# Kernel optimization log

Measured on AMD Instinct MI355X. Metric: run time of the kernel, lower is better.

Reference implementation:

```python
import jax, jax.numpy as jnp
import numpy as np

D_MODEL = 768
N_HEADS = 12
HEAD_DIM = D_MODEL // N_HEADS
FFN_DIM = 3072
MAX_WAVELENGTH = 10000.0
ROPE_PERCENT = 0.5
NORM_EPS = 1e-5


def setup_inputs() -> dict:
    key = jax.random.key(0)
    ks = jax.random.split(key, 12)
    B, C, S = 2, 16, 128
    init = lambda k, shape: (jax.random.normal(k, shape, dtype=jnp.float32) * 0.02)
    return {
        "hidden_state": jax.random.normal(ks[0], (B, C, S, D_MODEL), dtype=jnp.float32),
        "wq": init(ks[1], (D_MODEL, D_MODEL)), "bq": jnp.zeros((D_MODEL,), jnp.float32),
        "wk": init(ks[2], (D_MODEL, D_MODEL)), "bk": jnp.zeros((D_MODEL,), jnp.float32),
        "wv": init(ks[3], (D_MODEL, D_MODEL)), "bv": jnp.zeros((D_MODEL,), jnp.float32),
        "wo": init(ks[4], (D_MODEL, D_MODEL)), "bo": jnp.zeros((D_MODEL,), jnp.float32),
        "attn_biases": init(ks[5], (N_HEADS, 2)),
        "ln1_g": jnp.ones((D_MODEL,), jnp.float32), "ln1_b": jnp.zeros((D_MODEL,), jnp.float32),
        "ln3_g": jnp.ones((D_MODEL,), jnp.float32), "ln3_b": jnp.zeros((D_MODEL,), jnp.float32),
        "w1": init(ks[6], (D_MODEL, FFN_DIM)), "b1": jnp.zeros((FFN_DIM,), jnp.float32),
        "w2": init(ks[7], (FFN_DIM, D_MODEL)), "b2": jnp.zeros((D_MODEL,), jnp.float32),
    }


def _layernorm(x, g, b):
    mu = jnp.mean(x, axis=-1, keepdims=True)
    var = jnp.mean(jnp.square(x - mu), axis=-1, keepdims=True)
    return (x - mu) * jax.lax.rsqrt(var + NORM_EPS) * g + b


def _apply_p_rope(x, positions):
    # x: [B, H, T, head_dim]; p-RoPE: only rope_percent of frequency bands rotate.
    half = HEAD_DIM // 2
    rope_angles = int(ROPE_PERCENT * HEAD_DIM) // 2  # 16
    fraction = 2.0 * jnp.arange(rope_angles, dtype=jnp.float32) / HEAD_DIM
    timescale = jnp.concatenate([
        MAX_WAVELENGTH ** fraction,
        jnp.full((half - rope_angles,), jnp.inf, dtype=jnp.float32),
    ])  # [half]
    angles = positions[:, None].astype(jnp.float32) / timescale[None, :]  # [T, half]
    sin = jnp.sin(angles)[None, None]  # [1,1,T,half]
    cos = jnp.cos(angles)[None, None]
    x1, x2 = jnp.split(x, 2, axis=-1)
    return jnp.concatenate([x1 * cos - x2 * sin, x2 * cos + x1 * sin], axis=-1)


def _forward(hidden_state, wq, bq, wk, bk, wv, bv, wo, bo, attn_biases,
             ln1_g, ln1_b, ln3_g, ln3_b, w1, b1, w2, b2):
    B, C, S, D = hidden_state.shape
    T = C * S
    flat = hidden_state.reshape(B, T, D)

    # --- attention sublayer (pre-norm) ---
    ni = _layernorm(flat, ln1_g, ln1_b)
    scaling = HEAD_DIM ** -0.5
    q = (ni @ wq + bq) * scaling
    k = ni @ wk + bk
    v = ni @ wv + bv
    to_heads = lambda t: t.reshape(B, T, N_HEADS, HEAD_DIM).transpose(0, 2, 1, 3)
    q, k, v = to_heads(q), to_heads(k), to_heads(v)  # [B,H,T,hd]

    positions = jnp.arange(T)
    k = _apply_p_rope(k, positions)
    q = _apply_p_rope(q, positions)

    scores = jnp.einsum("bhtd,bhsd->bhts", q, k)  # [B,H,T,T]
    variate_ids = positions // S
    same = (variate_ids[:, None] == variate_ids[None, :]).astype(scores.dtype)  # [T,T]
    variate_bias = (same[None, :, :] * attn_biases[:, 0][:, None, None]
                    + (1.0 - same[None, :, :]) * attn_biases[:, 1][:, None, None])  # [H,T,T]
    scores = scores + variate_bias[None]
    probs = jax.nn.softmax(scores, axis=-1)
    attn = jnp.einsum("bhts,bhsd->bhtd", probs, v)
    attn = attn.transpose(0, 2, 1, 3).reshape(B, T, D)
    attn = attn @ wo + bo

    flat = flat + attn  # residual (pre-norm -> no post-norm here)

    # --- feed-forward sublayer (pre-norm) ---
    ff_in = _layernorm(flat, ln3_g, ln3_b)
    ff = jax.nn.gelu(ff_in @ w1 + b1, approximate=False) @ w2 + b2
    flat = flat + ff

    return flat.reshape(B, C, S, D)


def reference(hidden_state, wq, bq, wk, bk, wv, bv, wo, bo, attn_biases,
              ln1_g, ln1_b, ln3_g, ln3_b, w1, b1, w2, b2):
    return _forward(hidden_state, wq, bq, wk, bk, wv, bv, wo, bo, attn_biases,
                    ln1_g, ln1_b, ln3_g, ln3_b, w1, b1, w2, b2)
```

## Files before the change

### kernel.cpp

```cpp
#include <hip/hip_runtime.h>
#include <cmath>


typedef __bf16 bf16_t;
typedef bf16_t bf16x8 __attribute__((ext_vector_type(8)));
typedef float floatx4 __attribute__((ext_vector_type(4)));
typedef unsigned int u32x4 __attribute__((ext_vector_type(4)));

#define MFMA(a, b, c) __builtin_amdgcn_mfma_f32_16x16x32_bf16((a), (b), (c), 0, 0, 0)
#define LOG2E 1.44269504088896340736f

__device__ __forceinline__ bf16_t f2bf(float f) { return (bf16_t)f; }

__device__ __forceinline__ void g2l16(const void* g, void* l) {
  __builtin_amdgcn_global_load_lds(
      (const __attribute__((address_space(1))) unsigned int*)g,
      (__attribute__((address_space(3))) unsigned int*)l, 16, 0, 0);
}

__device__ __forceinline__ void wait_vm4() {
  asm volatile("s_waitcnt vmcnt(4)" ::: "memory");
}
__device__ __forceinline__ void wait_vm0() {
  asm volatile("s_waitcnt vmcnt(0)" ::: "memory");
}

__device__ __forceinline__ unsigned cvt_pk_bf16(float lo, float hi) {
  unsigned r;
  asm("v_cvt_pk_bf16_f32 %0, %1, %2" : "=v"(r) : "v"(lo), "v"(hi));
  return r;
}
__device__ __forceinline__ void pl32swap(unsigned& a, unsigned& b) {
  asm("v_permlane32_swap_b32 %0, %1" : "+v"(a), "+v"(b));
}
__device__ __forceinline__ void pl16swap(unsigned& a, unsigned& b) {
  asm("v_permlane16_swap_b32 %0, %1" : "+v"(a), "+v"(b));
}

struct PrepP {
  const float *wq, *wk, *wv, *wo, *w1, *w2;
  bf16_t *wqkvT, *woT, *w1T, *w2T;
  const float *hs, *g1, *be1;
  bf16_t* ni;
};

__global__ __launch_bounds__(256) void k_prep(PrepP p) {
  __shared__ float shm[32 * 33];
  const int bid = blockIdx.x;
  if (bid < 6912) {
    const float* in;
    bf16_t* out;
    int R, C, tx, ty;
    if (bid < 2304) {
      int m = bid / 576, lo = bid % 576;
      in = (m == 0) ? p.wq : (m == 1) ? p.wk : (m == 2) ? p.wv : p.wo;
      out = (m < 3) ? p.wqkvT + (size_t)m * 768 * 768 : p.woT;
      R = 768; C = 768; tx = lo % 24; ty = lo / 24;
    } else if (bid < 4608) {
      int lo = bid - 2304;
      in = p.w1; out = p.w1T; R = 768; C = 3072; tx = lo % 96; ty = lo / 96;
    } else {
      int lo = bid - 4608;
      in = p.w2; out = p.w2T; R = 3072; C = 768; tx = lo % 24; ty = lo / 24;
    }
    const int c0 = tx * 32, r0 = ty * 32;
    const int lx = threadIdx.x & 31, ly = threadIdx.x >> 5;
#pragma unroll
    for (int p4 = 0; p4 < 4; p4++) {
      int r = ly + p4 * 8;
      shm[r * 33 + lx] = in[(size_t)(r0 + r) * C + c0 + lx];
    }
    __syncthreads();
#pragma unroll
    for (int p4 = 0; p4 < 4; p4++) {
      int r = ly + p4 * 8;
      out[(size_t)(c0 + r) * R + r0 + lx] = f2bf(shm[lx * 33 + r]);
    }
  } else {
    const int row = bid - 6912;
    const float* xr = p.hs + (size_t)row * 768;
    const int t = threadIdx.x;
    float v0 = xr[t], v1 = xr[t + 256], v2 = xr[t + 512];
    float s = v0 + v1 + v2;
    float s2 = v0 * v0 + v1 * v1 + v2 * v2;
#pragma unroll
    for (int off = 32; off; off >>= 1) {
      s += __shfl_xor(s, off);
      s2 += __shfl_xor(s2, off);
    }
    const int w = t >> 6;
    if ((t & 63) == 0) { shm[w] = s; shm[4 + w] = s2; }
    __syncthreads();
    s = shm[0] + shm[1] + shm[2] + shm[3];
    s2 = shm[4] + shm[5] + shm[6] + shm[7];
    const float mu = s * (1.0f / 768.0f);
    const float var = s2 * (1.0f / 768.0f) - mu * mu;
    const float rstd = rsqrtf(var + 1e-5f);
    bf16_t* orow = p.ni + (size_t)row * 768;
    orow[t]       = f2bf((v0 - mu) * rstd * p.g1[t]       + p.be1[t]);
    orow[t + 256] = f2bf((v1 - mu) * rstd * p.g1[t + 256] + p.be1[t + 256]);
    orow[t + 512] = f2bf((v2 - mu) * rstd * p.g1[t + 512] + p.be1[t + 512]);
  }
}

__global__ __launch_bounds__(256) void k_layernorm(
    const float* __restrict__ x, const float* __restrict__ g,
    const float* __restrict__ b, bf16_t* __restrict__ out) {
  const int row = blockIdx.x;
  const float* xr = x + (size_t)row * 768;
  const int t = threadIdx.x;
  float v0 = xr[t], v1 = xr[t + 256], v2 = xr[t + 512];
  float s = v0 + v1 + v2;
  float s2 = v0 * v0 + v1 * v1 + v2 * v2;
#pragma unroll
  for (int off = 32; off; off >>= 1) {
    s += __shfl_xor(s, off);
    s2 += __shfl_xor(s2, off);
  }
  __shared__ float ra[4], rb[4];
  const int w = t >> 6;
  if ((t & 63) == 0) { ra[w] = s; rb[w] = s2; }
  __syncthreads();
  s = ra[0] + ra[1] + ra[2] + ra[3];
  s2 = rb[0] + rb[1] + rb[2] + rb[3];
  const float mu = s * (1.0f / 768.0f);
  const float var = s2 * (1.0f / 768.0f) - mu * mu;
  const float rstd = rsqrtf(var + 1e-5f);
  bf16_t* orow = out + (size_t)row * 768;
  orow[t]       = f2bf((v0 - mu) * rstd * g[t]       + b[t]);
  orow[t + 256] = f2bf((v1 - mu) * rstd * g[t + 256] + b[t + 256]);
  orow[t + 512] = f2bf((v2 - mu) * rstd * g[t + 512] + b[t + 512]);
}

struct GemmP {
  const bf16_t* A;
  const bf16_t* Bt;
  int M, N, K, mode;
  const float* bias0;
  const float* bias1;
  const float* bias2;
  float* outF;
  bf16_t* outB0;
  bf16_t* outB1;
  bf16_t* outB2;
};

__global__ __launch_bounds__(256, 3) void k_gemm(GemmP p) {
  __shared__ bf16_t lds[18432];
  const int tid = threadIdx.x;
  const int lane = tid & 63, wave = tid >> 6;
  const int quad = lane >> 4, l15 = lane & 15;
  const int wm = (wave >> 1) * 64, wn = (wave & 1) * 64;
  const int m0 = blockIdx.y * 128, n0 = blockIdx.x * 128;

  const char* gA[4];
  const char* gB[4];
#pragma unroll
  for (int pp = 0; pp < 4; pp++) {
    int slot = wave * 256 + pp * 64 + lane;
    int r = slot >> 3;
    int c8 = ((slot & 7) ^ (r & 7)) << 3;
    gA[pp] = (const char*)(p.A + (size_t)(m0 + r) * p.K + c8);
    gB[pp] = (const char*)(p.Bt + (size_t)(n0 + r) * p.K + c8);
  }

  int offA[4], offB[4];
#pragma unroll
  for (int i = 0; i < 4; i++) {
    int ra = wm + i * 16 + l15;
    offA[i] = ra * 64 + ((quad * 8) ^ ((ra & 7) << 3));
    int rb = wn + i * 16 + l15;
    offB[i] = rb * 64 + ((quad * 8) ^ ((rb & 7) << 3));
  }

  const floatx4 z4 = {0.f, 0.f, 0.f, 0.f};
  floatx4 acc[4][4];
#pragma unroll
  for (int i = 0; i < 4; i++)
#pragma unroll
    for (int j = 0; j < 4; j++) acc[i][j] = z4;

  const int KT = p.K >> 6;
  bf16_t* Ad = lds + wave * 2048;
  bf16_t* Bd = lds + 8192 + wave * 2048;

  for (int kt = 0; kt < KT; kt++) {
    const size_t kb = (size_t)kt * 128;
#pragma unroll
    for (int pp = 0; pp < 4; pp++) {
      g2l16(gA[pp] + kb, Ad + pp * 512);
      g2l16(gB[pp] + kb, Bd + pp * 512);
    }
    __syncthreads();
#pragma unroll
    for (int ks = 0; ks < 2; ks++) {
      bf16x8 af[4], bfr[4];
#pragma unroll
      for (int i = 0; i < 4; i++) {
        af[i] = *(const bf16x8*)(lds + (offA[i] ^ (ks * 32)));
        bfr[i] = *(const bf16x8*)(lds + 8192 + (offB[i] ^ (ks * 32)));
      }
#pragma unroll
      for (int i = 0; i < 4; i++)
#pragma unroll
        for (int j = 0; j < 4; j++) acc[i][j] = MFMA(af[i], bfr[j], acc[i][j]);
    }
    __syncthreads();
  }

  char* scr = (char*)lds + wave * 9216;

  if (p.mode == 0) {
    const int gnw = n0 + wn;
    const int region = gnw / 768;
    const int rem = gnw - region * 768;
    const int h = rem >> 6;
    const int b = (m0 + wm) >> 11;
    const int t0 = (m0 + wm) & 2047;
    const float* bias = (region == 0) ? p.bias0 : (region == 1 ? p.bias1 : p.bias2);
    float bb[4];
#pragma unroll
    for (int j = 0; j < 4; j++) bb[j] = bias[h * 64 + j * 16 + l15];
    bf16_t* sb = (bf16_t*)scr;
    if (region < 2) {
      const float scale = (region == 0) ? 0.125f * LOG2E : 1.0f;
      const float inv_ts = exp2f(-(float)l15 * (13.287712379549449f / 32.0f));
#pragma unroll
      for (int i = 0; i < 4; i++) {
#pragma unroll
        for (int reg = 0; reg < 4; reg++) {
          int tl = i * 16 + quad * 4 + reg;
          float sn, cs;
          __sincosf((float)(t0 + tl) * inv_ts, &sn, &cs);
          float v0 = (acc[i][0][reg] + bb[0]) * scale;
          float v1 = (acc[i][1][reg] + bb[1]) * scale;
          float v2 = (acc[i][2][reg] + bb[2]) * scale;
          float v3 = (acc[i][3][reg] + bb[3]) * scale;
          sb[tl * 72 + l15]      = f2bf(v0 * cs - v2 * sn);
          sb[tl * 72 + 16 + l15] = f2bf(v1);
          sb[tl * 72 + 32 + l15] = f2bf(v2 * cs + v0 * sn);
          sb[tl * 72 + 48 + l15] = f2bf(v3);
        }
      }
      __syncthreads();
      bf16_t* outp = (region == 0) ? p.outB0 : p.outB1;
      bf16_t* ob = outp + (((size_t)(b * 12 + h) * 2048 + t0) << 6);
#pragma unroll
      for (int pp = 0; pp < 8; pp++) {
        int row = pp * 8 + (lane >> 3), ch = (lane & 7) << 3;
        *(bf16x8*)(ob + row * 64 + ch) = *(const bf16x8*)&sb[row * 72 + ch];
      }
    } else {
#pragma unroll
      for (int i = 0; i < 4; i++)
#pragma unroll
        for (int j = 0; j < 4; j++)
#pragma unroll
          for (int reg = 0; reg < 4; reg++)
            sb[(j * 16 + l15) * 72 + i * 16 + quad * 4 + reg] =
                f2bf(acc[i][j][reg] + bb[j]);
      __syncthreads();
      bf16_t* ob = p.outB2 + (((size_t)(b * 12 + h)) << 17) + t0;
#pragma unroll
      for (int pp = 0; pp < 8; pp++) {
        int d = pp * 8 + (lane >> 3), ch = (lane & 7) << 3;
        *(bf16x8*)(ob + (size_t)d * 2048 + ch) = *(const bf16x8*)&sb[d * 72 + ch];
      }
    }
  } else {
    bf16_t* sb = (bf16_t*)scr;
    float bb[4];
#pragma unroll
    for (int j = 0; j < 4; j++) bb[j] = p.bias0[n0 + wn + j * 16 + l15];
#pragma unroll
    for (int i = 0; i < 4; i++)
#pragma unroll
      for (int j = 0; j < 4; j++)
#pragma unroll
        for (int reg = 0; reg < 4; reg++) {
          int tl = i * 16 + quad * 4 + reg;
          float x = acc[i][j][reg] + bb[j];
          float gv = 0.5f * x * (1.0f + erff(x * 0.70710678118654752f));
          sb[tl * 72 + j * 16 + l15] = f2bf(gv);
        }
    __syncthreads();
#pragma unroll
    for (int pp = 0; pp < 8; pp++) {
      int row = pp * 8 + (lane >> 3), ch = (lane & 7) << 3;
      *(bf16x8*)(p.outB0 + (size_t)(m0 + wm + row) * p.N + n0 + wn + ch) =
          *(const bf16x8*)&sb[row * 72 + ch];
    }
  }
}

__global__ __launch_bounds__(256, 4) void k_gemm64(
    const bf16_t* __restrict__ A, const bf16_t* __restrict__ Bt, int N, int K,
    const float* __restrict__ bias, const float* __restrict__ resid,
    float* __restrict__ outF) {
  __shared__ bf16_t lds[16384];
  const int tid = threadIdx.x;
  const int lane = tid & 63, wave = tid >> 6;
  const int quad = lane >> 4, l15 = lane & 15;
  const int wm = (wave >> 1) * 32, wn = (wave & 1) * 32;
  const int m0 = blockIdx.y * 64, n0 = blockIdx.x * 64;

  const char* gA[4];
  const char* gB[4];
#pragma unroll
  for (int pp = 0; pp < 4; pp++) {
    int slot = wave * 256 + pp * 64 + lane;
    int r = slot >> 4;
    int c = ((slot & 15) ^ (r & 7)) << 3;
    gA[pp] = (const char*)(A + (size_t)(m0 + r) * K + c);
    gB[pp] = (const char*)(Bt + (size_t)(n0 + r) * K + c);
  }

  const floatx4 z4 = {0.f, 0.f, 0.f, 0.f};
  floatx4 acc[2][2];
#pragma unroll
  for (int i = 0; i < 2; i++)
#pragma unroll
    for (int j = 0; j < 2; j++) acc[i][j] = z4;

  const int KT = K >> 7;
  bf16_t* Ad = lds + wave * 2048;
  bf16_t* Bd = lds + 8192 + wave * 2048;

  for (int kt = 0; kt < KT; kt++) {
    const size_t kb = (size_t)kt * 256;
#pragma unroll
    for (int pp = 0; pp < 4; pp++) {
      g2l16(gA[pp] + kb, Ad + pp * 512);
      g2l16(gB[pp] + kb, Bd + pp * 512);
    }
    __syncthreads();
#pragma unroll
    for (int ks = 0; ks < 4; ks++) {
      bf16x8 af[2], bfr[2];
#pragma unroll
      for (int i = 0; i < 2; i++) {
        int ra = wm + i * 16 + l15;
        af[i] = *(const bf16x8*)(lds + ra * 128 +
                                 (((ks * 4 + quad) ^ (ra & 7)) << 3));
        int rb = wn + i * 16 + l15;
        bfr[i] = *(const bf16x8*)(lds + 8192 + rb * 128 +
                                  (((ks * 4 + quad) ^ (rb & 7)) << 3));
      }
#pragma unroll
      for (int i = 0; i < 2; i++)
#pragma unroll
        for (int j = 0; j < 2; j++) acc[i][j] = MFMA(af[i], bfr[j], acc[i][j]);
    }
    __syncthreads();
  }

  float* s4 = (float*)lds + wave * 1024;
#pragma unroll
  for (int i = 0; i < 2; i++)
#pragma unroll
    for (int j = 0; j < 2; j++)
#pragma unroll
      for (int reg = 0; reg < 4; reg++)
        s4[(i * 16 + quad * 4 + reg) * 32 + j * 16 + l15] = acc[i][j][reg];
  __syncthreads();
#pragma unroll
  for (int pp = 0; pp < 4; pp++) {
    int row = pp * 8 + (lane >> 3);
    int c4 = (lane & 7) * 4;
    floatx4 v = *(const floatx4*)&s4[row * 32 + c4];
    size_t goff = (size_t)(m0 + wm + row) * N + n0 + wn + c4;
    floatx4 rv = *(const floatx4*)(resid + goff);
    floatx4 bv = *(const floatx4*)(bias + n0 + wn + c4);
    *(floatx4*)(outF + goff) = v + rv + bv;
  }
}

__global__ __launch_bounds__(256, 3) void k_flash(
    const bf16_t* __restrict__ qh, const bf16_t* __restrict__ kh,
    const bf16_t* __restrict__ vt, const float* __restrict__ ab,
    bf16_t* __restrict__ attnA) {
  __shared__ bf16_t sm[25088];

  const int tid = threadIdx.x, lane = tid & 63, wave = tid >> 6;
  const int quad = lane >> 4, l15 = lane & 15;
  const int qtile = blockIdx.x, bh = blockIdx.y;
  const int h = bh % 12, bq = bh / 12;
  const int myv = qtile >> 1;

  bf16_t* wb = sm + wave * 6144;
  bf16_t* Kb0 = wb;
  bf16_t* Vs = wb + 2048;

  const bf16_t* Qg = qh + ((size_t)bh * 2048 + qtile * 64) * 64;
  const bf16_t* Kg = kh + ((size_t)bh * 2048 + wave * 16) * 64;

  const char* gK[2];
#pragma unroll
  for (int i = 0; i < 2; i++) {
    int sl = i * 8 + (lane >> 3);
    int cs = (lane & 7) ^ (sl & 7);
    gK[i] = (const char*)(Kg + sl * 64 + cs * 8);
  }
  const char* gV[2];
#pragma unroll
  for (int i = 0; i < 2; i++) {
    int d = i * 32 + (lane >> 1);
    int hs = (lane & 1) ^ ((d >> 2) & 1);
    gV[i] = (const char*)(vt + ((size_t)(bh * 64 + d)) * 2048 + wave * 16 + hs * 8);
  }

  bf16x8 qf[4][2];
#pragma unroll
  for (int mt = 0; mt < 4; mt++)
#pragma unroll
    for (int ks = 0; ks < 2; ks++)
      qf[mt][ks] = *(const bf16x8*)(Qg + (size_t)(mt * 16 + l15) * 64 +
                                    ks * 32 + quad * 8);

  int offKr[2];
#pragma unroll
  for (int ks = 0; ks < 2; ks++)
    offKr[ks] = l15 * 64 + ((((ks << 2) + quad) ^ (l15 & 7)) << 3);
  int offV[4];
#pragma unroll
  for (int nt = 0; nt < 4; nt++) {
    int d = nt * 16 + l15;
    offV[nt] = (quad >> 1) * 1024 + d * 16 +
               (((quad & 1) ^ ((d >> 2) & 1)) << 3);
  }

  const floatx4 z4 = {0.f, 0.f, 0.f, 0.f};
  floatx4 oacc[4][4];
  float l_mt[4];
  unsigned pA[4], pB[4];
#pragma unroll
  for (int mt = 0; mt < 4; mt++)
#pragma unroll
    for (int nt = 0; nt < 4; nt++) oacc[mt][nt] = z4;
#pragma unroll
  for (int mt = 0; mt < 4; mt++) l_mt[mt] = 0.f;

  const float bc_same = ab[h * 2] * LOG2E;
  const float bc_diff = ab[h * 2 + 1] * LOG2E;

  g2l16(gK[0], Kb0);
  g2l16(gK[1], Kb0 + 512);
  g2l16(gV[0], Vs);
  g2l16(gV[1], Vs + 512);

#pragma unroll 2
  for (int kv = 0; kv < 32; kv++) {
    const int nkv = (kv + 1) & 31;
    {
      const size_t kbK = (size_t)nkv * 8192, kbV = (size_t)nkv * 128;
      bf16_t* Kd = Kb0 + (nkv & 1) * 1024;
      bf16_t* Vd = Vs + ((((nkv >> 1) & 1) << 1) + (nkv & 1)) * 1024;
      g2l16(gK[0] + kbK, Kd);
      g2l16(gK[1] + kbK, Kd + 512);
      g2l16(gV[0] + kbV, Vd);
      g2l16(gV[1] + kbV, Vd + 512);
    }
    wait_vm4();

    const bf16_t* Kc = Kb0 + (kv & 1) * 1024;
    const float bc = ((kv >> 1) == myv) ? bc_same : bc_diff;
    floatx4 sacc[4];
#pragma unroll
    for (int mt = 0; mt < 4; mt++) sacc[mt] = (floatx4){bc, bc, bc, bc};
#pragma unroll
    for (int ks = 0; ks < 2; ks++) {
      const bf16x8 kf = *(const bf16x8*)(Kc + offKr[ks]);
#pragma unroll
      for (int mt = 0; mt < 4; mt++)
        sacc[mt] = MFMA(kf, qf[mt][ks], sacc[mt]);
    }

    if (!(kv & 1)) {
#pragma unroll
      for (int mt = 0; mt < 4; mt++) {
        float p0 = exp2f(sacc[mt][0]), p1 = exp2f(sacc[mt][1]);
        float p2 = exp2f(sacc[mt][2]), p3 = exp2f(sacc[mt][3]);
        l_mt[mt] += (p0 + p1) + (p2 + p3);
        pA[mt] = cvt_pk_bf16(p0, p1);
        pB[mt] = cvt_pk_bf16(p2, p3);
      }
    } else {
      bf16x8 vf[4];
      const int vb = ((kv >> 1) & 1) * 2048;
#pragma unroll
      for (int nt = 0; nt < 4; nt++)
        vf[nt] = *(const bf16x8*)(Vs + vb + offV[nt]);
#pragma unroll
      for (int mt = 0; mt < 4; mt++) {
        float p0 = exp2f(sacc[mt][0]), p1 = exp2f(sacc[mt][1]);
        float p2 = exp2f(sacc[mt][2]), p3 = exp2f(sacc[mt][3]);
        l_mt[mt] += (p0 + p1) + (p2 + p3);
        unsigned b0 = cvt_pk_bf16(p0, p1);
        unsigned b1 = cvt_pk_bf16(p2, p3);
        unsigned a0 = pA[mt], a1 = pB[mt];
        pl32swap(a0, b0);
        pl16swap(a0, b0);
        pl32swap(a1, b1);
        pl16swap(a1, b1);
        u32x4 w;
        w[0] = a0; w[1] = a1; w[2] = b0; w[3] = b1;
        const bf16x8 pf = __builtin_bit_cast(bf16x8, w);
#pragma unroll
        for (int nt = 0; nt < 4; nt++)
          oacc[mt][nt] = MFMA(pf, vf[nt], oacc[mt][nt]);
      }
    }
  }

  wait_vm0();

#pragma unroll
  for (int mt = 0; mt < 4; mt++) {
    float v = l_mt[mt];
    v += __shfl_xor(v, 16);
    v += __shfl_xor(v, 32);
    l_mt[mt] = v;
  }
  float* lred = (float*)(sm + 24576);
  if (quad == 0) {
#pragma unroll
    for (int mt = 0; mt < 4; mt++)
      lred[wave * 64 + mt * 16 + l15] = l_mt[mt];
  }
#pragma unroll
  for (int mt = 0; mt < 4; mt++)
#pragma unroll
    for (int nt = 0; nt < 4; nt++)
#pragma unroll
      for (int reg = 0; reg < 4; reg++)
        wb[(mt * 16 + quad * 4 + reg) * 64 + nt * 16 + l15] =
            f2bf(oacc[mt][nt][reg]);
  __syncthreads();

  const int q = tid >> 2, dg = (tid & 3) * 16;
  const float inv =
      1.0f / (lred[q] + lred[64 + q] + lred[128 + q] + lred[192 + q]);
  float o[16];
#pragma unroll
  for (int j = 0; j < 16; j++) o[j] = 0.f;
#pragma unroll
  for (int w = 0; w < 4; w++) {
    const bf16x8 a = *(const bf16x8*)(sm + w * 6144 + q * 64 + dg);
    const bf16x8 b = *(const bf16x8*)(sm + w * 6144 + q * 64 + dg + 8);
#pragma unroll
    for (int j = 0; j < 8; j++) {
      o[j] += (float)a[j];
      o[8 + j] += (float)b[j];
    }
  }
  bf16x8 r0, r1;
#pragma unroll
  for (int j = 0; j < 8; j++) {
    r0[j] = f2bf(o[j] * inv);
    r1[j] = f2bf(o[8 + j] * inv);
  }
  bf16_t* outp =
      attnA + ((size_t)(bq * 2048 + qtile * 64 + q)) * 768 + h * 64 + dg;
  *(bf16x8*)outp = r0;
  *(bf16x8*)(outp + 8) = r1;
}

extern "C" void kernel_launch(void* const* d_in, const int* in_sizes, int n_in,
                              void* d_out, int out_size, void* d_ws,
                              size_t ws_size, hipStream_t stream) {
  const float* hs  = (const float*)d_in[0];
  const float* wq  = (const float*)d_in[1];
  const float* bq  = (const float*)d_in[2];
  const float* wk  = (const float*)d_in[3];
  const float* bk  = (const float*)d_in[4];
  const float* wv  = (const float*)d_in[5];
  const float* bv  = (const float*)d_in[6];
  const float* wo  = (const float*)d_in[7];
  const float* bo  = (const float*)d_in[8];
  const float* ab  = (const float*)d_in[9];
  const float* g1  = (const float*)d_in[10];
  const float* be1 = (const float*)d_in[11];
  const float* g3  = (const float*)d_in[12];
  const float* be3 = (const float*)d_in[13];
  const float* w1  = (const float*)d_in[14];
  const float* b1  = (const float*)d_in[15];
  const float* w2  = (const float*)d_in[16];
  const float* b2  = (const float*)d_in[17];

  char* ws = (char*)d_ws;
  size_t off = 0;
  auto alloc = [&](size_t bytes) -> void* {
    void* p = ws + off;
    off += (bytes + 255) & ~(size_t)255;
    return p;
  };
  bf16_t* wqkvT = (bf16_t*)alloc((size_t)2304 * 768 * 2);
  bf16_t* woT   = (bf16_t*)alloc((size_t)768 * 768 * 2);
  bf16_t* w1T   = (bf16_t*)alloc((size_t)3072 * 768 * 2);
  bf16_t* w2T   = (bf16_t*)alloc((size_t)768 * 3072 * 2);
  bf16_t* ni    = (bf16_t*)alloc((size_t)4096 * 768 * 2);
  bf16_t* qhB   = (bf16_t*)alloc((size_t)24 * 2048 * 64 * 2);
  bf16_t* khB   = (bf16_t*)alloc((size_t)24 * 2048 * 64 * 2);
  bf16_t* vtB   = (bf16_t*)alloc((size_t)24 * 64 * 2048 * 2);
  bf16_t* attnA = (bf16_t*)alloc((size_t)4096 * 768 * 2);
  float*  resid1 = (float*)alloc((size_t)4096 * 768 * 4);
  bf16_t* ffn1o = qhB;

  PrepP pp = {wq, wk, wv, wo, w1, w2, wqkvT, woT, w1T, w2T, hs, g1, be1, ni};
  k_prep<<<11008, 256, 0, stream>>>(pp);

  GemmP gqkv = {ni, wqkvT, 4096, 2304, 768, 0,
                bq, bk, bv, nullptr, qhB, khB, vtB};
  k_gemm<<<dim3(18, 32), 256, 0, stream>>>(gqkv);

  k_flash<<<dim3(32, 24), 256, 0, stream>>>(qhB, khB, vtB, ab, attnA);

  k_gemm64<<<dim3(12, 64), 256, 0, stream>>>(attnA, woT, 768, 768, bo, hs,
                                             resid1);

  k_layernorm<<<4096, 256, 0, stream>>>(resid1, g3, be3, ni);

  GemmP gf1 = {ni, w1T, 4096, 3072, 768, 2,
               b1, nullptr, nullptr, nullptr, ffn1o, nullptr, nullptr};
  k_gemm<<<dim3(24, 32), 256, 0, stream>>>(gf1);

  k_gemm64<<<dim3(12, 64), 256, 0, stream>>>(ffn1o, w2T, 768, 3072, b2,
                                             resid1, (float*)d_out);
}
```

Baseline: 269.2 us.

## Load V fragments directly to registers and deepen K prefetch in flash kernel

The flash-attention kernel stops staging V through LDS. Each wave now loads V fragments straight from global memory into double-buffered registers one pair-iteration ahead, while K is prefetched two steps ahead in a four-slot LDS ring. The variate bias is restructured to initialize scores with the cross-variate bias and multiply by a precomputed exp2 ratio on same-variate tiles, and it uses the raw hardware exp2 builtin. Less LDS per block may allow higher occupancy, but the change adds register pressure and exposes direct global-load latency for V.

```diff
diff --git a/kernel.cpp b/kernel.cpp
--- a/kernel.cpp
+++ b/kernel.cpp
@@ -12,14 +12,18 @@
 
 __device__ __forceinline__ bf16_t f2bf(float f) { return (bf16_t)f; }
 
+__device__ __forceinline__ float fexp2(float x) {
+  return __builtin_amdgcn_exp2f(x);
+}
+
 __device__ __forceinline__ void g2l16(const void* g, void* l) {
   __builtin_amdgcn_global_load_lds(
       (const __attribute__((address_space(1))) unsigned int*)g,
       (__attribute__((address_space(3))) unsigned int*)l, 16, 0, 0);
 }
 
-__device__ __forceinline__ void wait_vm4() {
-  asm volatile("s_waitcnt vmcnt(4)" ::: "memory");
+__device__ __forceinline__ void wait_vm8() {
+  asm volatile("s_waitcnt vmcnt(8)" ::: "memory");
 }
 __device__ __forceinline__ void wait_vm0() {
   asm volatile("s_waitcnt vmcnt(0)" ::: "memory");
@@ -379,7 +383,7 @@
     const bf16_t* __restrict__ qh, const bf16_t* __restrict__ kh,
     const bf16_t* __restrict__ vt, const float* __restrict__ ab,
     bf16_t* __restrict__ attnA) {
-  __shared__ bf16_t sm[25088];
+  __shared__ bf16_t sm[16896];
 
   const int tid = threadIdx.x, lane = tid & 63, wave = tid >> 6;
   const int quad = lane >> 4, l15 = lane & 15;
@@ -387,9 +391,7 @@
   const int h = bh % 12, bq = bh / 12;
   const int myv = qtile >> 1;
 
-  bf16_t* wb = sm + wave * 6144;
-  bf16_t* Kb0 = wb;
-  bf16_t* Vs = wb + 2048;
+  bf16_t* wb = sm + wave * 4096;
 
   const bf16_t* Qg = qh + ((size_t)bh * 2048 + qtile * 64) * 64;
   const bf16_t* Kg = kh + ((size_t)bh * 2048 + wave * 16) * 64;
@@ -401,13 +403,12 @@
     int cs = (lane & 7) ^ (sl & 7);
     gK[i] = (const char*)(Kg + sl * 64 + cs * 8);
   }
-  const char* gV[2];
-#pragma unroll
-  for (int i = 0; i < 2; i++) {
-    int d = i * 32 + (lane >> 1);
-    int hs = (lane & 1) ^ ((d >> 2) & 1);
-    gV[i] = (const char*)(vt + ((size_t)(bh * 64 + d)) * 2048 + wave * 16 + hs * 8);
-  }
+
+  int voff[4];
+#pragma unroll
+  for (int nt = 0; nt < 4; nt++)
+    voff[nt] = (bh * 64 + nt * 16 + l15) * 2048 + wave * 16 +
+               (quad >> 1) * 64 + (quad & 1) * 8;
 
   bf16x8 qf[4][2];
 #pragma unroll
@@ -421,13 +422,6 @@
 #pragma unroll
   for (int ks = 0; ks < 2; ks++)
     offKr[ks] = l15 * 64 + ((((ks << 2) + quad) ^ (l15 & 7)) << 3);
-  int offV[4];
-#pragma unroll
-  for (int nt = 0; nt < 4; nt++) {
-    int d = nt * 16 + l15;
-    offV[nt] = (quad >> 1) * 1024 + d * 16 +
-               (((quad & 1) ^ ((d >> 2) & 1)) << 3);
-  }
 
   const floatx4 z4 = {0.f, 0.f, 0.f, 0.f};
   floatx4 oacc[4][4];
@@ -442,75 +436,89 @@
 
   const float bc_same = ab[h * 2] * LOG2E;
   const float bc_diff = ab[h * 2 + 1] * LOG2E;
-
-  g2l16(gK[0], Kb0);
-  g2l16(gK[1], Kb0 + 512);
-  g2l16(gV[0], Vs);
-  g2l16(gV[1], Vs + 512);
-
-#pragma unroll 2
-  for (int kv = 0; kv < 32; kv++) {
-    const int nkv = (kv + 1) & 31;
-    {
-      const size_t kbK = (size_t)nkv * 8192, kbV = (size_t)nkv * 128;
-      bf16_t* Kd = Kb0 + (nkv & 1) * 1024;
-      bf16_t* Vd = Vs + ((((nkv >> 1) & 1) << 1) + (nkv & 1)) * 1024;
-      g2l16(gK[0] + kbK, Kd);
-      g2l16(gK[1] + kbK, Kd + 512);
-      g2l16(gV[0] + kbV, Vd);
-      g2l16(gV[1] + kbV, Vd + 512);
-    }
-    wait_vm4();
-
-    const bf16_t* Kc = Kb0 + (kv & 1) * 1024;
-    const float bc = ((kv >> 1) == myv) ? bc_same : bc_diff;
-    floatx4 sacc[4];
-#pragma unroll
-    for (int mt = 0; mt < 4; mt++) sacc[mt] = (floatx4){bc, bc, bc, bc};
-#pragma unroll
-    for (int ks = 0; ks < 2; ks++) {
-      const bf16x8 kf = *(const bf16x8*)(Kc + offKr[ks]);
-#pragma unroll
-      for (int mt = 0; mt < 4; mt++)
-        sacc[mt] = MFMA(kf, qf[mt][ks], sacc[mt]);
-    }
-
-    if (!(kv & 1)) {
-#pragma unroll
-      for (int mt = 0; mt < 4; mt++) {
-        float p0 = exp2f(sacc[mt][0]), p1 = exp2f(sacc[mt][1]);
-        float p2 = exp2f(sacc[mt][2]), p3 = exp2f(sacc[mt][3]);
-        l_mt[mt] += (p0 + p1) + (p2 + p3);
-        pA[mt] = cvt_pk_bf16(p0, p1);
-        pB[mt] = cvt_pk_bf16(p2, p3);
-      }
-    } else {
-      bf16x8 vf[4];
-      const int vb = ((kv >> 1) & 1) * 2048;
-#pragma unroll
-      for (int nt = 0; nt < 4; nt++)
-        vf[nt] = *(const bf16x8*)(Vs + vb + offV[nt]);
-#pragma unroll
-      for (int mt = 0; mt < 4; mt++) {
-        float p0 = exp2f(sacc[mt][0]), p1 = exp2f(sacc[mt][1]);
-        float p2 = exp2f(sacc[mt][2]), p3 = exp2f(sacc[mt][3]);
-        l_mt[mt] += (p0 + p1) + (p2 + p3);
-        unsigned b0 = cvt_pk_bf16(p0, p1);
-        unsigned b1 = cvt_pk_bf16(p2, p3);
-        unsigned a0 = pA[mt], a1 = pB[mt];
-        pl32swap(a0, b0);
-        pl16swap(a0, b0);
-        pl32swap(a1, b1);
-        pl16swap(a1, b1);
-        u32x4 w;
-        w[0] = a0; w[1] = a1; w[2] = b0; w[3] = b1;
-        const bf16x8 pf = __builtin_bit_cast(bf16x8, w);
-#pragma unroll
-        for (int nt = 0; nt < 4; nt++)
-          oacc[mt][nt] = MFMA(pf, vf[nt], oacc[mt][nt]);
-      }
-    }
-  }
+  const float ratio = fexp2(bc_same - bc_diff);
+  const floatx4 bD4 = {bc_diff, bc_diff, bc_diff, bc_diff};
+
+  g2l16(gK[0], wb);
+  g2l16(gK[1], wb + 512);
+  g2l16(gK[0] + 8192, wb + 1024);
+  g2l16(gK[1] + 8192, wb + 1024 + 512);
+  bf16x8 vfA[4], vfB[4];
+#pragma unroll
+  for (int nt = 0; nt < 4; nt++) vfA[nt] = *(const bf16x8*)(vt + voff[nt]);
+
+#define PAIR_BODY(PJ, VCUR, VNEXT)                                           \
+  {                                                                          \
+    const int kve = 2 * (PJ), kvo = kve + 1;                                 \
+    const int kn0 = (kve + 2) & 31, kn1 = (kvo + 2) & 31;                    \
+    g2l16(gK[0] + (size_t)kn0 * 8192, wb + (kn0 & 3) * 1024);                \
+    g2l16(gK[1] + (size_t)kn0 * 8192, wb + (kn0 & 3) * 1024 + 512);          \
+    g2l16(gK[0] + (size_t)kn1 * 8192, wb + (kn1 & 3) * 1024);                \
+    g2l16(gK[1] + (size_t)kn1 * 8192, wb + (kn1 & 3) * 1024 + 512);          \
+    const int vadd = (((PJ) + 1) & 15) * 128;                                \
+    _Pragma("unroll")                                                        \
+    for (int nt = 0; nt < 4; nt++)                                           \
+      VNEXT[nt] = *(const bf16x8*)(vt + voff[nt] + vadd);                    \
+    wait_vm8();                                                              \
+    const bool same = ((PJ) == myv);                                         \
+    {                                   \
+      const bf16_t* Kc = wb + (kve & 3) * 1024;                              \
+      const bf16x8 kf0 = *(const bf16x8*)(Kc + offKr[0]);                    \
+      const bf16x8 kf1 = *(const bf16x8*)(Kc + offKr[1]);                    \
+      floatx4 se[4];                                                         \
+      _Pragma("unroll")                                                      \
+      for (int mt = 0; mt < 4; mt++) {                                       \
+        se[mt] = MFMA(kf0, qf[mt][0], bD4);                                  \
+        se[mt] = MFMA(kf1, qf[mt][1], se[mt]);                               \
+      }                                                                      \
+      _Pragma("unroll")                                                      \
+      for (int mt = 0; mt < 4; mt++) {                                       \
+        float p0 = fexp2(se[mt][0]), p1 = fexp2(se[mt][1]);                  \
+        float p2 = fexp2(se[mt][2]), p3 = fexp2(se[mt][3]);                  \
+        if (same) { p0 *= ratio; p1 *= ratio; p2 *= ratio; p3 *= ratio; }    \
+        l_mt[mt] += (p0 + p1) + (p2 + p3);                                   \
+        pA[mt] = cvt_pk_bf16(p0, p1);                                        \
+        pB[mt] = cvt_pk_bf16(p2, p3);                                        \
+      }                                                                      \
+    }                                                                        \
+    {                   \
+      const bf16_t* Kc = wb + (kvo & 3) * 1024;                              \
+      const bf16x8 kf0 = *(const bf16x8*)(Kc + offKr[0]);                    \
+      const bf16x8 kf1 = *(const bf16x8*)(Kc + offKr[1]);                    \
+      floatx4 so[4];                                                         \
+      _Pragma("unroll")                                                      \
+      for (int mt = 0; mt < 4; mt++) {                                       \
+        so[mt] = MFMA(kf0, qf[mt][0], bD4);                                  \
+        so[mt] = MFMA(kf1, qf[mt][1], so[mt]);                               \
+      }                                                                      \
+      _Pragma("unroll")                                                      \
+      for (int mt = 0; mt < 4; mt++) {                                       \
+        float p0 = fexp2(so[mt][0]), p1 = fexp2(so[mt][1]);                  \
+        float p2 = fexp2(so[mt][2]), p3 = fexp2(so[mt][3]);                  \
+        if (same) { p0 *= ratio; p1 *= ratio; p2 *= ratio; p3 *= ratio; }    \
+        l_mt[mt] += (p0 + p1) + (p2 + p3);                                   \
+        unsigned b0 = cvt_pk_bf16(p0, p1);                                   \
+        unsigned b1 = cvt_pk_bf16(p2, p3);                                   \
+        unsigned a0 = pA[mt], a1 = pB[mt];                                   \
+        pl32swap(a0, b0);                                                    \
+        pl16swap(a0, b0);                                                    \
+        pl32swap(a1, b1);                                                    \
+        pl16swap(a1, b1);                                                    \
+        u32x4 wr;                                                            \
+        wr[0] = a0; wr[1] = a1; wr[2] = b0; wr[3] = b1;                      \
+        const bf16x8 pf = __builtin_bit_cast(bf16x8, wr);                    \
+        _Pragma("unroll")                                                    \
+        for (int nt = 0; nt < 4; nt++)                                       \
+          oacc[mt][nt] = MFMA(pf, VCUR[nt], oacc[mt][nt]);                   \
+      }                                                                      \
+    }                                                                        \
+  }
+
+  for (int pj = 0; pj < 16; pj += 2) {
+    PAIR_BODY(pj, vfA, vfB);
+    PAIR_BODY(pj + 1, vfB, vfA);
+  }
+#undef PAIR_BODY
 
   wait_vm0();
 
@@ -521,7 +529,7 @@
     v += __shfl_xor(v, 32);
     l_mt[mt] = v;
   }
-  float* lred = (float*)(sm + 24576);
+  float* lred = (float*)(sm + 16384);
   if (quad == 0) {
 #pragma unroll
     for (int mt = 0; mt < 4; mt++)
@@ -545,8 +553,8 @@
   for (int j = 0; j < 16; j++) o[j] = 0.f;
 #pragma unroll
   for (int w = 0; w < 4; w++) {
-    const bf16x8 a = *(const bf16x8*)(sm + w * 6144 + q * 64 + dg);
-    const bf16x8 b = *(const bf16x8*)(sm + w * 6144 + q * 64 + dg + 8);
+    const bf16x8 a = *(const bf16x8*)(sm + w * 4096 + q * 64 + dg);
+    const bf16x8 b = *(const bf16x8*)(sm + w * 4096 + q * 64 + dg + 8);
 #pragma unroll
     for (int j = 0; j < 8; j++) {
       o[j] += (float)a[j];
```

Result: slower. 334.0 us (+24.1%).
